# Kernel tuning notes

Measured on AMD Instinct MI355X. Metric: run time of the kernel, lower is better.

The kernel has to match this reference:

```python
import jax, jax.numpy as jnp
import numpy as np

N_NODES = 100000
N_EDGES = 3200000
N_GRAPHS = 128
HIDDEN = 128
DEPTH = 3


def setup_inputs() -> dict:
    key = jax.random.key(0)
    ks = jax.random.split(key, 12)
    x = jax.random.normal(ks[0], (N_NODES, 1), dtype=jnp.float32)
    edge_index = jax.random.randint(ks[1], (2, N_EDGES), 0, N_NODES, dtype=jnp.int64)
    batch = jnp.sort(jax.random.randint(ks[2], (N_NODES,), 0, N_GRAPHS, dtype=jnp.int64))
    s = 1.0 / np.sqrt(HIDDEN)
    return {
        "x": x,
        "edge_index": edge_index,
        "batch": batch,
        "W_emb": jax.random.normal(ks[3], (1, HIDDEN), dtype=jnp.float32),
        "b_emb": jax.random.normal(ks[4], (HIDDEN,), dtype=jnp.float32) * 0.01,
        "W_gnn": jax.random.normal(ks[5], (DEPTH, HIDDEN, HIDDEN), dtype=jnp.float32) * s,
        "b_gnn": jax.random.normal(ks[6], (DEPTH, HIDDEN), dtype=jnp.float32) * 0.01,
        "W_c1": jax.random.normal(ks[7], (HIDDEN, HIDDEN // 2), dtype=jnp.float32) * s,
        "b_c1": jax.random.normal(ks[8], (HIDDEN // 2,), dtype=jnp.float32) * 0.01,
        "W_c2": jax.random.normal(ks[9], (HIDDEN // 2, 1), dtype=jnp.float32) * s,
        "b_c2": jax.random.normal(ks[10], (1,), dtype=jnp.float32) * 0.01,
    }


def reference(x, edge_index, batch, W_emb, b_emb, W_gnn, b_gnn, W_c1, b_c1, W_c2, b_c2):
    # --- GCN normalization (self-loops + symmetric deg^-1/2) ---
    loop = jnp.arange(N_NODES, dtype=edge_index.dtype)
    row = jnp.concatenate([edge_index[0], loop])  # source nodes
    col = jnp.concatenate([edge_index[1], loop])  # target nodes
    deg = jax.ops.segment_sum(jnp.ones_like(col, dtype=jnp.float32), col, num_segments=N_NODES)
    dinv = jnp.where(deg > 0, jax.lax.rsqrt(jnp.maximum(deg, 1.0)), 0.0)
    norm = dinv[row] * dinv[col]  # [E+N]

    # --- node embedding ---
    h = x @ W_emb + b_emb  # [N, H]

    # --- GCN layers: linear -> gather -> normalize -> scatter-add -> bias -> relu ---
    for l in range(DEPTH):
        h_lin = h @ W_gnn[l]                       # [N, H]
        msgs = h_lin[row] * norm[:, None]          # [E+N, H]
        agg = jax.ops.segment_sum(msgs, col, num_segments=N_NODES)
        h = jax.nn.relu(agg + b_gnn[l])

    # --- global mean pool per graph ---
    counts = jax.ops.segment_sum(jnp.ones((N_NODES,), jnp.float32), batch, num_segments=N_GRAPHS)
    sums = jax.ops.segment_sum(h, batch, num_segments=N_GRAPHS)
    g = sums / jnp.maximum(counts, 1.0)[:, None]   # [G, H]

    # --- classifier (dropout is identity in eval) ---
    z = jax.nn.relu(g @ W_c1 + b_c1)
    out = jax.nn.sigmoid(z @ W_c2 + b_c2)          # [G, 1]
    return out.squeeze(-1)                          # [G]
```

## Files before the change

### kernel.cpp

```cpp
#include <hip/hip_runtime.h>
#include <math.h>

#define HID 128
#define CAP 96
#define TILE 8192
#define WSH 9
#define BUKCAP 24576

typedef unsigned int uint;
typedef unsigned short ushort;
typedef float f32x2 __attribute__((ext_vector_type(2)));
typedef float f32x4 __attribute__((ext_vector_type(4)));
typedef short bf16x8 __attribute__((ext_vector_type(8)));

__device__ inline ushort f2bf(float f) {
    uint u = __float_as_uint(f);
    return (ushort)((u + 0x7fffu + ((u >> 16) & 1u)) >> 16);
}
__device__ inline uint packbf(float a, float b) {
    return (uint)f2bf(a) | ((uint)f2bf(b) << 16);
}

__device__ inline f32x2 fp8lo(uint q) { return __builtin_amdgcn_cvt_pk_f32_fp8(q, false); }
__device__ inline f32x2 fp8hi(uint q) { return __builtin_amdgcn_cvt_pk_f32_fp8(q, true); }
__device__ inline uint pack4fp8(float a, float b, float c, float d) {
    int t = __builtin_amdgcn_cvt_pk_fp8_f32(a, b, 0, false);
    return (uint)__builtin_amdgcn_cvt_pk_fp8_f32(c, d, t, true);
}
__device__ inline long long as_i64(uint2 u) {
    union { uint2 a; long long b; } c;
    c.a = u;
    return c.b;
}


__global__ void __launch_bounds__(256) k_part(const int* __restrict__ row,
                                              const int* __restrict__ col,
                                              int* __restrict__ bukCur,
                                              uint* __restrict__ recs, int E) {
    __shared__ int hist[256];
    __shared__ int hist2[256];
    __shared__ uint base[256];
    int t = threadIdx.x;
    hist[t] = 0;
    hist2[t] = 0;
    __syncthreads();
    int i0 = blockIdx.x * TILE;
    int i1 = min(E, i0 + TILE);
    for (int i = i0 + t; i < i1; i += 256) {
        int b = col[i] >> WSH;
        atomicAdd(&hist[b], 1);
    }
    __syncthreads();
    if (hist[t] > 0) base[t] = (uint)atomicAdd(&bukCur[t], hist[t]);
    __syncthreads();
    for (int i = i0 + t; i < i1; i += 256) {
        int c = col[i];
        int b = c >> WSH;
        uint p = (uint)atomicAdd(&hist2[b], 1);
        uint idx = base[b] + p;
        if (idx < BUKCAP)
            recs[(size_t)b * BUKCAP + idx] = (uint)row[i] | ((uint)(c & 511) << 17);
    }
}

__global__ void __launch_bounds__(256) k_fbin(const uint* __restrict__ recs,
                                              const int* __restrict__ bukCur,
                                              const float* __restrict__ x,
                                              int* __restrict__ cnt,
                                              int* __restrict__ ebin,
                                              float* __restrict__ dinv,
                                              float2* __restrict__ pk0, int N) {
    __shared__ int lcnt[128];
    int b = blockIdx.x >> 2;
    int q = blockIdx.x & 3;
    int t = threadIdx.x;
    if (t < 128) lcnt[t] = 0;
    __syncthreads();
    int n = min(bukCur[b], BUKCAP);
    const uint* rp = recs + (size_t)b * BUKCAP;
    int cbase = (b << WSH) + (q << 7);
    for (int j = t; j < n; j += 256) {
        uint u = rp[j];
        if ((int)(u >> 24) == q) {
            int r = (int)(u & 0x1FFFFu);
            int cl = (int)((u >> 17) & 127u);
            int p = atomicAdd(&lcnt[cl], 1);
            if (p < CAP) ebin[(size_t)(cbase + cl) * CAP + p] = r << 5;
        }
    }
    __syncthreads();
    if (t < 128) {
        int c = cbase + t;
        if (c < N) {
            cnt[c] = lcnt[t];
            float d = rsqrtf((float)lcnt[t] + 1.0f);
            dinv[c] = d;
            pk0[c] = make_float2(d, d * x[c]);
        }
    }
}


__global__ void k_wprep(const float* __restrict__ W_emb, const float* __restrict__ b_emb,
                        const float* __restrict__ W_gnn,
                        float* __restrict__ u, float* __restrict__ v,
                        uint2* __restrict__ wfrag) {
    int b = blockIdx.x;
    int t = threadIdx.x;
    if (b < 16) {
        int gid = b * 256 + t;
        int l = gid >> 11;
        int rem = gid & 2047;
        int kb = rem >> 9;
        int nt = (rem >> 6) & 7;
        int lane = rem & 63;
        int k0 = kb * 32 + (lane >> 4) * 8;
        int n = nt * 16 + (lane & 15);
        const float* Wp = W_gnn + (size_t)(l + 1) * HID * HID;
        uint2 o;
        o.x = pack4fp8(Wp[(k0 + 0) * HID + n], Wp[(k0 + 1) * HID + n],
                       Wp[(k0 + 2) * HID + n], Wp[(k0 + 3) * HID + n]);
        o.y = pack4fp8(Wp[(k0 + 4) * HID + n], Wp[(k0 + 5) * HID + n],
                       Wp[(k0 + 6) * HID + n], Wp[(k0 + 7) * HID + n]);
        wfrag[gid] = o;
    } else if (t < HID) {
        float su = 0.f, sv = 0.f;
        for (int k = 0; k < HID; ++k) {
            float w = W_gnn[k * HID + t];
            su = fmaf(W_emb[k], w, su);
            sv = fmaf(b_emb[k], w, sv);
        }
        u[t] = su;
        v[t] = sv;
    }
}


__global__ void __launch_bounds__(256) k_sagg(const int* __restrict__ cnt,
                                              const int* __restrict__ ebin,
                                              const float* __restrict__ x,
                                              const float* __restrict__ dinv,
                                              const float2* __restrict__ pk0,
                                              const float* __restrict__ u,
                                              const float* __restrict__ v,
                                              const float* __restrict__ b0,
                                              uint* __restrict__ g8, int N) {
    __shared__ float sS0[16], sS1[16], sDc[16];
    int t = threadIdx.x;
    int qw = t >> 4;
    int ll = t & 15;
    int c0 = blockIdx.x * 16;
    int c = c0 + qw;
    float A = 0.f, B = 0.f;
    float dc = 0.f;
    if (c < N) {
        dc = dinv[c];
        int n = min(cnt[c], CAP);
        const int* bp = ebin + (size_t)c * CAP;
        int k = ll;
        for (; k + 16 < n; k += 32) {
            int o0 = bp[k], o1 = bp[k + 16];
            float2 p0 = pk0[o0 >> 5], p1 = pk0[o1 >> 5];
            A += p0.x + p1.x;
            B += p0.y + p1.y;
        }
        if (k < n) {
            float2 p = pk0[bp[k] >> 5];
            A += p.x;
            B += p.y;
        }
    }
#pragma unroll
    for (int m = 1; m <= 8; m <<= 1) {
        A += __shfl_xor(A, m);
        B += __shfl_xor(B, m);
    }
    if (ll == 0 && c < N) {
        float d2 = dc * dc;
        sS0[qw] = fmaf(dc, A, d2);
        sS1[qw] = fmaf(dc, B, d2 * x[c]);
        sDc[qw] = dc;
    }
    __syncthreads();
    int nloc = min(16, N - c0);
    int total = nloc * 32;
    for (int gid = t; gid < total; gid += 256) {
        int lc = gid >> 5;
        int j = (gid & 31) * 4;
        float t1 = sS1[lc], t0 = sS0[lc], dcc = sDc[lc];
        float v0 = fmaxf(fmaf(t1, u[j + 0], fmaf(t0, v[j + 0], b0[j + 0])), 0.f);
        float v1 = fmaxf(fmaf(t1, u[j + 1], fmaf(t0, v[j + 1], b0[j + 1])), 0.f);
        float v2 = fmaxf(fmaf(t1, u[j + 2], fmaf(t0, v[j + 2], b0[j + 2])), 0.f);
        float v3 = fmaxf(fmaf(t1, u[j + 3], fmaf(t0, v[j + 3], b0[j + 3])), 0.f);
        g8[(size_t)(c0 + lc) * 32 + (gid & 31)] = pack4fp8(dcc * v0, dcc * v1, dcc * v2, dcc * v3);
    }
}


__global__ void __launch_bounds__(256) k_agg(const int* __restrict__ cnt,
                                             const int* __restrict__ ebin,
                                             const float* __restrict__ dinv,
                                             const uint* __restrict__ g8,
                                             uint* __restrict__ a, int N) {
    int wave = (blockIdx.x * 256 + threadIdx.x) >> 6;
    if (wave >= N) return;
    int lane = threadIdx.x & 63;
    int c = wave;
    int ql = lane & 15;
    int qg = lane >> 4;
    const uint* __restrict__ gq = g8 + ql * 2;

    f32x2 a0 = {0.f, 0.f}, a1 = {0.f, 0.f}, a2 = {0.f, 0.f}, a3 = {0.f, 0.f};

    int n = min(cnt[c], CAP);
    int total = n + 1;
    const int* __restrict__ bp = ebin + (size_t)c * CAP - 1;

    for (int base = 0; base < total; base += 64) {
        int cw = min(total - base, 64);
        int gi = base + lane;
        int ro = 0;
        if (lane < cw) ro = (gi == 0) ? (c << 5) : bp[gi];
        int j = 0;
        for (; j + 16 <= cw; j += 16) {
            int o0 = __shfl(ro, j + qg);
            int o1 = __shfl(ro, j + 4 + qg);
            int o2 = __shfl(ro, j + 8 + qg);
            int o3 = __shfl(ro, j + 12 + qg);
            uint2 q0 = *(const uint2*)(gq + o0);
            uint2 q1 = *(const uint2*)(gq + o1);
            uint2 q2 = *(const uint2*)(gq + o2);
            uint2 q3 = *(const uint2*)(gq + o3);
            a0 += fp8lo(q0.x); a1 += fp8hi(q0.x); a2 += fp8lo(q0.y); a3 += fp8hi(q0.y);
            a0 += fp8lo(q1.x); a1 += fp8hi(q1.x); a2 += fp8lo(q1.y); a3 += fp8hi(q1.y);
            a0 += fp8lo(q2.x); a1 += fp8hi(q2.x); a2 += fp8lo(q2.y); a3 += fp8hi(q2.y);
            a0 += fp8lo(q3.x); a1 += fp8hi(q3.x); a2 += fp8lo(q3.y); a3 += fp8hi(q3.y);
        }
        for (; j + 4 <= cw; j += 4) {
            int o0 = __shfl(ro, j + qg);
            uint2 q0 = *(const uint2*)(gq + o0);
            a0 += fp8lo(q0.x); a1 += fp8hi(q0.x); a2 += fp8lo(q0.y); a3 += fp8hi(q0.y);
        }
        if (j < cw) {
            int e = j + qg;
            int o0 = __shfl(ro, min(e, cw - 1));
            uint2 q0 = *(const uint2*)(gq + o0);
            if (e >= cw) { q0.x = 0u; q0.y = 0u; }
            a0 += fp8lo(q0.x); a1 += fp8hi(q0.x); a2 += fp8lo(q0.y); a3 += fp8hi(q0.y);
        }
    }

    float r0 = a0.x, r1 = a0.y, r2 = a1.x, r3 = a1.y;
    float r4 = a2.x, r5 = a2.y, r6 = a3.x, r7 = a3.y;
#pragma unroll
    for (int m = 16; m <= 32; m <<= 1) {
        r0 += __shfl_xor(r0, m); r1 += __shfl_xor(r1, m);
        r2 += __shfl_xor(r2, m); r3 += __shfl_xor(r3, m);
        r4 += __shfl_xor(r4, m); r5 += __shfl_xor(r5, m);
        r6 += __shfl_xor(r6, m); r7 += __shfl_xor(r7, m);
    }
    if (qg == 0) {
        float dc = dinv[c];
        uint2 o;
        o.x = pack4fp8(dc * r0, dc * r1, dc * r2, dc * r3);
        o.y = pack4fp8(dc * r4, dc * r5, dc * r6, dc * r7);
        ((uint2*)(a + (size_t)c * 32))[ql] = o;
    }
}


#define RCH 32
__global__ void __launch_bounds__(256, 2) k_gemm(const uint* __restrict__ A,
                                                 const uint2* __restrict__ wfrag,
                                                 const float* __restrict__ bias,
                                                 const float* __restrict__ rowscale,
                                                 uint* __restrict__ H8, int N) {
    __shared__ uint2 sAf[4][2][64];
    __shared__ float sEp[4][16][68];
    int t = threadIdx.x;
    int w = t >> 6;
    int lane = t & 63;
    int rowgrp = w >> 1;
    int colh = w & 1;

    uint2 Bf[4][4];
#pragma unroll
    for (int kb = 0; kb < 4; ++kb)
#pragma unroll
        for (int i = 0; i < 4; ++i)
            Bf[kb][i] = wfrag[(kb * 8 + colh * 4 + i) * 64 + lane];

    float4 bb = ((const float4*)bias)[colh * 16 + (lane & 15)];

    int nchunk = (N + RCH - 1) / RCH;
    for (int ch = blockIdx.x; ch < nchunk; ch += gridDim.x) {
        int r0 = ch * RCH;
        __syncthreads();
        {
            int i = t;
#pragma unroll
            for (int s = 0; s < 2; ++s, i += 256) {
                int kb = i >> 7;
                int rg = (i >> 6) & 1;
                int ln = i & 63;
                int gr = r0 + rg * 16 + (ln & 15);
                gr = min(gr, N - 1);
                sAf[kb][rg][ln] = ((const uint2*)(A + (size_t)gr * 32))[kb * 4 + (ln >> 4)];
            }
        }
        __syncthreads();

        f32x4 acc[4] = {{0.f, 0.f, 0.f, 0.f}, {0.f, 0.f, 0.f, 0.f},
                        {0.f, 0.f, 0.f, 0.f}, {0.f, 0.f, 0.f, 0.f}};
#pragma unroll
        for (int kb = 0; kb < 4; ++kb) {
            long long af = as_i64(sAf[kb][rowgrp][lane]);
#pragma unroll
            for (int i = 0; i < 4; ++i)
                acc[i] = __builtin_amdgcn_mfma_f32_16x16x32_fp8_fp8(af, as_i64(Bf[kb][i]),
                                                                    acc[i], 0, 0, 0);
        }

#pragma unroll
        for (int i = 0; i < 4; ++i) {
#pragma unroll
            for (int reg = 0; reg < 4; ++reg)
                sEp[w][(lane >> 4) * 4 + reg][i * 16 + (lane & 15)] = acc[i][reg];
        }
#pragma unroll
        for (int e = 0; e < 4; ++e) {
            int rr = (lane >> 4) + 4 * e;
            int cu = lane & 15;
            const float* sp = &sEp[w][rr][cu * 4];
            int rowg = r0 + rowgrp * 16 + rr;
            if (rowg < N) {
                float sc = rowscale ? rowscale[rowg] : 1.0f;
                float o0 = sc * fmaxf(sp[0] + bb.x, 0.f);
                float o1 = sc * fmaxf(sp[1] + bb.y, 0.f);
                float o2 = sc * fmaxf(sp[2] + bb.z, 0.f);
                float o3 = sc * fmaxf(sp[3] + bb.w, 0.f);
                H8[(size_t)rowg * 32 + colh * 16 + cu] = pack4fp8(o0, o1, o2, o3);
            }
        }
    }
}


__global__ void k_pool(const uint* __restrict__ h8, const int* __restrict__ batch,
                       float* __restrict__ gpool, float* __restrict__ gcnt, int N) {
    int gi = blockIdx.x >> 2, part = blockIdx.x & 3;
    int t = threadIdx.x;
    int ui = t & 31;
    int sub = t >> 5;
    int lo = 0, hi = N;
    while (lo < hi) { int m = (lo + hi) >> 1; if (batch[m] < gi) lo = m + 1; else hi = m; }
    int start = lo;
    lo = start; hi = N;
    while (lo < hi) { int m = (lo + hi) >> 1; if (batch[m] <= gi) lo = m + 1; else hi = m; }
    int end = lo;
    if (part == 0 && t == 0) gcnt[gi] = (float)(end - start);
    int len = end - start;
    int q = (len + 15) >> 4;
    int seg = part * 4 + sub;
    int rs = start + seg * q;
    int re = min(end, rs + q);
    float s0 = 0.f, s1 = 0.f, s2 = 0.f, s3 = 0.f;
    for (int i = rs; i < re; ++i) {
        uint qq = h8[(size_t)i * 32 + ui];
        f32x2 lo2 = fp8lo(qq), hi2 = fp8hi(qq);
        s0 += lo2.x; s1 += lo2.y; s2 += hi2.x; s3 += hi2.y;
    }
    if (re > rs) {
        float* gp = gpool + gi * HID + ui * 4;
        atomicAdd(gp + 0, s0);
        atomicAdd(gp + 1, s1);
        atomicAdd(gp + 2, s2);
        atomicAdd(gp + 3, s3);
    }
}

__global__ void k_cls(const float* __restrict__ gpool, const float* __restrict__ gcnt,
                      const float* __restrict__ Wc1, const float* __restrict__ bc1,
                      const float* __restrict__ Wc2, const float* __restrict__ bc2,
                      float* __restrict__ out) {
    int g = blockIdx.x;
    int j = threadIdx.x;
    float inv = 1.0f / fmaxf(gcnt[g], 1.0f);
    float z = bc1[j];
    for (int k = 0; k < HID; ++k) z = fmaf(gpool[g * HID + k] * inv, Wc1[k * 64 + j], z);
    z = fmaxf(z, 0.f);
    float p = z * Wc2[j];
    for (int off = 32; off; off >>= 1) p += __shfl_down(p, off);
    if (j == 0) out[g] = 1.0f / (1.0f + expf(-(p + bc2[0])));
}


extern "C" void kernel_launch(void* const* d_in, const int* in_sizes, int n_in,
                              void* d_out, int out_size, void* d_ws, size_t ws_size,
                              hipStream_t stream) {
    const float* x     = (const float*)d_in[0];
    const int*   eidx  = (const int*)d_in[1];
    const int*   batch = (const int*)d_in[2];
    const float* W_emb = (const float*)d_in[3];
    const float* b_emb = (const float*)d_in[4];
    const float* W_gnn = (const float*)d_in[5];
    const float* b_gnn = (const float*)d_in[6];
    const float* W_c1  = (const float*)d_in[7];
    const float* b_c1  = (const float*)d_in[8];
    const float* W_c2  = (const float*)d_in[9];
    const float* b_c2  = (const float*)d_in[10];

    const int N = in_sizes[0];
    const int E = in_sizes[1] / 2;
    const int G = out_size;
    const int* row = eidx;
    const int* col = eidx + E;
    const int NBUK = (N + 511) >> WSH;

    char* ws = (char*)d_ws;
    auto alloc = [&](size_t bytes) -> void* {
        void* p = (void*)ws;
        ws += (bytes + 255) & ~(size_t)255;
        return p;
    };
    int*    cnt    = (int*)alloc((size_t)N * 4);
    float*  dinv   = (float*)alloc((size_t)N * 4);
    float2* pk0    = (float2*)alloc((size_t)N * 8);
    int*    bukCur = (int*)alloc(256 * 4);
    uint*   recs   = (uint*)alloc((size_t)NBUK * BUKCAP * 4);
    int*    ebin   = (int*)alloc((size_t)N * CAP * 4);
    float*  u      = (float*)alloc(HID * 4);
    float*  v      = (float*)alloc(HID * 4);
    uint*   G8     = (uint*)alloc((size_t)N * 32 * 4);
    uint*   A      = (uint*)alloc((size_t)N * 32 * 4);
    uint2*  wfrag  = (uint2*)alloc(4096 * 8);
    float*  gpool  = (float*)alloc((size_t)G * HID * 4);
    float*  gcnt   = (float*)alloc((size_t)G * 4);

    hipMemsetAsync(bukCur, 0, 256 * 4, stream);
    hipMemsetAsync(gpool, 0, (size_t)G * HID * 4, stream);

    k_part<<<(E + TILE - 1) / TILE, 256, 0, stream>>>(row, col, bukCur, recs, E);
    k_fbin<<<NBUK * 4, 256, 0, stream>>>(recs, bukCur, x, cnt, ebin, dinv, pk0, N);

    k_wprep<<<17, 256, 0, stream>>>(W_emb, b_emb, W_gnn, u, v, wfrag);

    k_sagg<<<(N + 15) / 16, 256, 0, stream>>>(cnt, ebin, x, dinv, pk0, u, v, b_gnn, G8, N);

    int nchunk = (N + RCH - 1) / RCH;
    int gblk = nchunk < 768 ? nchunk : 768;
    for (int l = 1; l < 3; ++l) {
        k_agg<<<(N + 3) / 4, 256, 0, stream>>>(cnt, ebin, dinv, G8, A, N);
        k_gemm<<<gblk, 256, 0, stream>>>(A, wfrag + (size_t)(l - 1) * 2048,
                                         b_gnn + (size_t)l * HID,
                                         (l == 1) ? dinv : (const float*)nullptr,
                                         G8, N);
    }

    k_pool<<<G * 4, 128, 0, stream>>>(G8, batch, gpool, gcnt, N);
    k_cls<<<G, 64, 0, stream>>>(gpool, gcnt, W_c1, b_c1, W_c2, b_c2, (float*)d_out);
}
```

Baseline: 361.2 us.

## Partition edges directly into 128-node windows and fuse weight prep and pooling setup

The edge partition now buckets by 128-node windows (782 buckets) instead of 512-node buckets, so each k_fbin block reads only its own window rather than four blocks each scanning a whole bucket and filtering. Weight fragment preparation is folded into extra blocks of k_part, removing one launch. Pooling writes per-part partial sums through shared memory instead of global atomics, and the classifier sums them, which removes a memset. The trade-offs are an 800-entry shared histogram with more atomic contention spread, and a per-window capacity of 6144 records that could overflow on skewed graphs.

```diff
diff --git a/kernel.cpp b/kernel.cpp
--- a/kernel.cpp
+++ b/kernel.cpp
@@ -4,8 +4,7 @@
 #define HID 128
 #define CAP 96
 #define TILE 8192
-#define WSH 9
-#define BUKCAP 24576
+#define WCAP 6144
 
 typedef unsigned int uint;
 typedef unsigned short ushort;
@@ -37,32 +36,67 @@
 __global__ void __launch_bounds__(256) k_part(const int* __restrict__ row,
                                               const int* __restrict__ col,
                                               int* __restrict__ bukCur,
-                                              uint* __restrict__ recs, int E) {
-    __shared__ int hist[256];
-    __shared__ int hist2[256];
-    __shared__ uint base[256];
+                                              uint* __restrict__ recs, int E, int nTiles,
+                                              const float* __restrict__ W_emb,
+                                              const float* __restrict__ b_emb,
+                                              const float* __restrict__ W_gnn,
+                                              float* __restrict__ u, float* __restrict__ v,
+                                              uint2* __restrict__ wfrag) {
+    __shared__ int hist[800];
+    __shared__ int hist2[800];
+    __shared__ uint base[800];
     int t = threadIdx.x;
-    hist[t] = 0;
-    hist2[t] = 0;
+    if ((int)blockIdx.x >= nTiles) {
+        int b = blockIdx.x - nTiles;
+        if (b < 16) {
+            int gid = b * 256 + t;
+            int l = gid >> 11;
+            int rem = gid & 2047;
+            int kb = rem >> 9;
+            int nt = (rem >> 6) & 7;
+            int lane = rem & 63;
+            int k0 = kb * 32 + (lane >> 4) * 8;
+            int n = nt * 16 + (lane & 15);
+            const float* Wp = W_gnn + (size_t)(l + 1) * HID * HID;
+            uint2 o;
+            o.x = pack4fp8(Wp[(k0 + 0) * HID + n], Wp[(k0 + 1) * HID + n],
+                           Wp[(k0 + 2) * HID + n], Wp[(k0 + 3) * HID + n]);
+            o.y = pack4fp8(Wp[(k0 + 4) * HID + n], Wp[(k0 + 5) * HID + n],
+                           Wp[(k0 + 6) * HID + n], Wp[(k0 + 7) * HID + n]);
+            wfrag[gid] = o;
+        } else if (t < HID) {
+            float su = 0.f, sv = 0.f;
+            for (int k = 0; k < HID; ++k) {
+                float w = W_gnn[k * HID + t];
+                su = fmaf(W_emb[k], w, su);
+                sv = fmaf(b_emb[k], w, sv);
+            }
+            u[t] = su;
+            v[t] = sv;
+        }
+        return;
+    }
+    for (int i = t; i < 800; i += 256) { hist[i] = 0; hist2[i] = 0; }
     __syncthreads();
     int i0 = blockIdx.x * TILE;
     int i1 = min(E, i0 + TILE);
     for (int i = i0 + t; i < i1; i += 256) {
-        int b = col[i] >> WSH;
-        atomicAdd(&hist[b], 1);
-    }
-    __syncthreads();
-    if (hist[t] > 0) base[t] = (uint)atomicAdd(&bukCur[t], hist[t]);
+        atomicAdd(&hist[col[i] >> 7], 1);
+    }
+    __syncthreads();
+    for (int i = t; i < 800; i += 256)
+        if (hist[i] > 0) base[i] = (uint)atomicAdd(&bukCur[i], hist[i]);
     __syncthreads();
     for (int i = i0 + t; i < i1; i += 256) {
         int c = col[i];
-        int b = c >> WSH;
-        uint p = (uint)atomicAdd(&hist2[b], 1);
-        uint idx = base[b] + p;
-        if (idx < BUKCAP)
-            recs[(size_t)b * BUKCAP + idx] = (uint)row[i] | ((uint)(c & 511) << 17);
-    }
-}
+        int w = c >> 7;
+        uint p = (uint)atomicAdd(&hist2[w], 1);
+        uint idx = base[w] + p;
+        if (idx < WCAP)
+            recs[(size_t)w * WCAP + idx] = (uint)row[i] | ((uint)(c & 127) << 17);
+    }
+}
+
 
 __global__ void __launch_bounds__(256) k_fbin(const uint* __restrict__ recs,
                                               const int* __restrict__ bukCur,
@@ -72,22 +106,19 @@
                                               float* __restrict__ dinv,
                                               float2* __restrict__ pk0, int N) {
     __shared__ int lcnt[128];
-    int b = blockIdx.x >> 2;
-    int q = blockIdx.x & 3;
+    int w = blockIdx.x;
     int t = threadIdx.x;
     if (t < 128) lcnt[t] = 0;
     __syncthreads();
-    int n = min(bukCur[b], BUKCAP);
-    const uint* rp = recs + (size_t)b * BUKCAP;
-    int cbase = (b << WSH) + (q << 7);
+    int n = min(bukCur[w], WCAP);
+    const uint* rp = recs + (size_t)w * WCAP;
+    int cbase = w << 7;
     for (int j = t; j < n; j += 256) {
         uint u = rp[j];
-        if ((int)(u >> 24) == q) {
-            int r = (int)(u & 0x1FFFFu);
-            int cl = (int)((u >> 17) & 127u);
-            int p = atomicAdd(&lcnt[cl], 1);
-            if (p < CAP) ebin[(size_t)(cbase + cl) * CAP + p] = r << 5;
-        }
+        int r = (int)(u & 0x1FFFFu);
+        int cl = (int)((u >> 17) & 127u);
+        int p = atomicAdd(&lcnt[cl], 1);
+        if (p < CAP) ebin[(size_t)(cbase + cl) * CAP + p] = r << 5;
     }
     __syncthreads();
     if (t < 128) {
@@ -98,41 +129,6 @@
             dinv[c] = d;
             pk0[c] = make_float2(d, d * x[c]);
         }
-    }
-}
-
-
-__global__ void k_wprep(const float* __restrict__ W_emb, const float* __restrict__ b_emb,
-                        const float* __restrict__ W_gnn,
-                        float* __restrict__ u, float* __restrict__ v,
-                        uint2* __restrict__ wfrag) {
-    int b = blockIdx.x;
-    int t = threadIdx.x;
-    if (b < 16) {
-        int gid = b * 256 + t;
-        int l = gid >> 11;
-        int rem = gid & 2047;
-        int kb = rem >> 9;
-        int nt = (rem >> 6) & 7;
-        int lane = rem & 63;
-        int k0 = kb * 32 + (lane >> 4) * 8;
-        int n = nt * 16 + (lane & 15);
-        const float* Wp = W_gnn + (size_t)(l + 1) * HID * HID;
-        uint2 o;
-        o.x = pack4fp8(Wp[(k0 + 0) * HID + n], Wp[(k0 + 1) * HID + n],
-                       Wp[(k0 + 2) * HID + n], Wp[(k0 + 3) * HID + n]);
-        o.y = pack4fp8(Wp[(k0 + 4) * HID + n], Wp[(k0 + 5) * HID + n],
-                       Wp[(k0 + 6) * HID + n], Wp[(k0 + 7) * HID + n]);
-        wfrag[gid] = o;
-    } else if (t < HID) {
-        float su = 0.f, sv = 0.f;
-        for (int k = 0; k < HID; ++k) {
-            float w = W_gnn[k * HID + t];
-            su = fmaf(W_emb[k], w, su);
-            sv = fmaf(b_emb[k], w, sv);
-        }
-        u[t] = su;
-        v[t] = sv;
     }
 }
 
@@ -347,12 +343,17 @@
 }
 
 
+
 __global__ void k_pool(const uint* __restrict__ h8, const int* __restrict__ batch,
-                       float* __restrict__ gpool, float* __restrict__ gcnt, int N) {
+                       float* __restrict__ gpp, float* __restrict__ gcnt, int N) {
+    __shared__ float sp[128];
     int gi = blockIdx.x >> 2, part = blockIdx.x & 3;
+    int G = gridDim.x >> 2;
     int t = threadIdx.x;
     int ui = t & 31;
     int sub = t >> 5;
+    sp[t] = 0.f;
+    __syncthreads();
     int lo = 0, hi = N;
     while (lo < hi) { int m = (lo + hi) >> 1; if (batch[m] < gi) lo = m + 1; else hi = m; }
     int start = lo;
@@ -372,23 +373,31 @@
         s0 += lo2.x; s1 += lo2.y; s2 += hi2.x; s3 += hi2.y;
     }
     if (re > rs) {
-        float* gp = gpool + gi * HID + ui * 4;
-        atomicAdd(gp + 0, s0);
-        atomicAdd(gp + 1, s1);
-        atomicAdd(gp + 2, s2);
-        atomicAdd(gp + 3, s3);
-    }
-}
-
-__global__ void k_cls(const float* __restrict__ gpool, const float* __restrict__ gcnt,
+        atomicAdd(&sp[ui * 4 + 0], s0);
+        atomicAdd(&sp[ui * 4 + 1], s1);
+        atomicAdd(&sp[ui * 4 + 2], s2);
+        atomicAdd(&sp[ui * 4 + 3], s3);
+    }
+    __syncthreads();
+    gpp[((size_t)part * G + gi) * 128 + t] = sp[t];
+}
+
+__global__ void k_cls(const float* __restrict__ gpp, const float* __restrict__ gcnt,
                       const float* __restrict__ Wc1, const float* __restrict__ bc1,
                       const float* __restrict__ Wc2, const float* __restrict__ bc2,
-                      float* __restrict__ out) {
+                      float* __restrict__ out, int G) {
+    __shared__ float sg[128];
     int g = blockIdx.x;
     int j = threadIdx.x;
     float inv = 1.0f / fmaxf(gcnt[g], 1.0f);
+    for (int k = j; k < 128; k += 64) {
+        float s = gpp[((size_t)0 * G + g) * 128 + k] + gpp[((size_t)1 * G + g) * 128 + k] +
+                  gpp[((size_t)2 * G + g) * 128 + k] + gpp[((size_t)3 * G + g) * 128 + k];
+        sg[k] = s * inv;
+    }
+    __syncthreads();
     float z = bc1[j];
-    for (int k = 0; k < HID; ++k) z = fmaf(gpool[g * HID + k] * inv, Wc1[k * 64 + j], z);
+    for (int k = 0; k < HID; ++k) z = fmaf(sg[k], Wc1[k * 64 + j], z);
     z = fmaxf(z, 0.f);
     float p = z * Wc2[j];
     for (int off = 32; off; off >>= 1) p += __shfl_down(p, off);
@@ -416,7 +425,7 @@
     const int G = out_size;
     const int* row = eidx;
     const int* col = eidx + E;
-    const int NBUK = (N + 511) >> WSH;
+    const int NWIN = (N + 127) >> 7;
 
     char* ws = (char*)d_ws;
     auto alloc = [&](size_t bytes) -> void* {
@@ -427,24 +436,23 @@
     int*    cnt    = (int*)alloc((size_t)N * 4);
     float*  dinv   = (float*)alloc((size_t)N * 4);
     float2* pk0    = (float2*)alloc((size_t)N * 8);
-    int*    bukCur = (int*)alloc(256 * 4);
-    uint*   recs   = (uint*)alloc((size_t)NBUK * BUKCAP * 4);
+    int*    bukCur = (int*)alloc((size_t)NWIN * 4);
+    uint*   recs   = (uint*)alloc((size_t)NWIN * WCAP * 4);
     int*    ebin   = (int*)alloc((size_t)N * CAP * 4);
     float*  u      = (float*)alloc(HID * 4);
     float*  v      = (float*)alloc(HID * 4);
     uint*   G8     = (uint*)alloc((size_t)N * 32 * 4);
     uint*   A      = (uint*)alloc((size_t)N * 32 * 4);
     uint2*  wfrag  = (uint2*)alloc(4096 * 8);
-    float*  gpool  = (float*)alloc((size_t)G * HID * 4);
+    float*  gpp    = (float*)alloc((size_t)4 * G * HID * 4);
     float*  gcnt   = (float*)alloc((size_t)G * 4);
 
-    hipMemsetAsync(bukCur, 0, 256 * 4, stream);
-    hipMemsetAsync(gpool, 0, (size_t)G * HID * 4, stream);
-
-    k_part<<<(E + TILE - 1) / TILE, 256, 0, stream>>>(row, col, bukCur, recs, E);
-    k_fbin<<<NBUK * 4, 256, 0, stream>>>(recs, bukCur, x, cnt, ebin, dinv, pk0, N);
-
-    k_wprep<<<17, 256, 0, stream>>>(W_emb, b_emb, W_gnn, u, v, wfrag);
+    hipMemsetAsync(bukCur, 0, (size_t)NWIN * 4, stream);
+
+    int nTiles = (E + TILE - 1) / TILE;
+    k_part<<<nTiles + 17, 256, 0, stream>>>(row, col, bukCur, recs, E, nTiles,
+                                            W_emb, b_emb, W_gnn, u, v, wfrag);
+    k_fbin<<<NWIN, 256, 0, stream>>>(recs, bukCur, x, cnt, ebin, dinv, pk0, N);
 
     k_sagg<<<(N + 15) / 16, 256, 0, stream>>>(cnt, ebin, x, dinv, pk0, u, v, b_gnn, G8, N);
 
@@ -458,6 +466,6 @@
                                          G8, N);
     }
 
-    k_pool<<<G * 4, 128, 0, stream>>>(G8, batch, gpool, gcnt, N);
-    k_cls<<<G, 64, 0, stream>>>(gpool, gcnt, W_c1, b_c1, W_c2, b_c2, (float*)d_out);
-}
+    k_pool<<<G * 4, 128, 0, stream>>>(G8, batch, gpp, gcnt, N);
+    k_cls<<<G, 64, 0, stream>>>(gpp, gcnt, W_c1, b_c1, W_c2, b_c2, (float*)d_out, G);
+}
```

Result: faster. 351.4 us (-2.7%).
